# Optimization experiments

Hardware: AMD Instinct MI355X
Metric: run time of the kernel (lower is better)

Reference implementation:

```python
import jax, jax.numpy as jnp
import numpy as np

N = 4096
IN_DIM = 6
HID = 32
HEADS1 = 4
OUT_DIM = 64


def _gat_layer(x, mask, W, a_src, a_dst, b):
    # x: [n, in], W: [in, heads*d], a_src/a_dst: [heads, d], b: [heads*d]
    n = x.shape[0]
    heads, d = a_src.shape
    h = (x @ W).reshape(n, heads, d)                      # [n, heads, d]
    e_src = jnp.einsum('nhd,hd->nh', h, a_src)            # [n, heads]
    e_dst = jnp.einsum('nhd,hd->nh', h, a_dst)            # [n, heads]
    logits = e_src[:, None, :] + e_dst[None, :, :]        # [n, n, heads]
    logits = jax.nn.leaky_relu(logits, negative_slope=0.2)
    logits = jnp.where(mask[:, :, None], logits, jnp.float32(-1e9))
    alpha = jax.nn.softmax(logits, axis=1)                # softmax over j (dim=1)
    # dropout disabled (eval mode reference)
    out = jnp.einsum('ijh,jhd->ihd', alpha, h).reshape(n, heads * d)
    return out + b


def setup_inputs() -> dict:
    key = jax.random.key(0)
    ks = jax.random.split(key, 10)
    x = jax.random.normal(ks[0], (N, IN_DIM), dtype=jnp.float32)
    adj = jax.random.bernoulli(ks[1], 0.01, (N, N)).astype(jnp.float32)
    s = 0.1
    W1 = jax.random.normal(ks[2], (IN_DIM, HEADS1 * HID), dtype=jnp.float32) * s
    a_src1 = jax.random.normal(ks[3], (HEADS1, HID), dtype=jnp.float32) * s
    a_dst1 = jax.random.normal(ks[4], (HEADS1, HID), dtype=jnp.float32) * s
    b1 = jnp.zeros((HEADS1 * HID,), dtype=jnp.float32)
    W2 = jax.random.normal(ks[5], (HEADS1 * HID, OUT_DIM), dtype=jnp.float32) * s
    a_src2 = jax.random.normal(ks[6], (1, OUT_DIM), dtype=jnp.float32) * s
    a_dst2 = jax.random.normal(ks[7], (1, OUT_DIM), dtype=jnp.float32) * s
    b2 = jnp.zeros((OUT_DIM,), dtype=jnp.float32)
    return {'x': x, 'adj': adj, 'W1': W1, 'a_src1': a_src1, 'a_dst1': a_dst1,
            'b1': b1, 'W2': W2, 'a_src2': a_src2, 'a_dst2': a_dst2, 'b2': b2}


def reference(x, adj, W1, a_src1, a_dst1, b1, W2, a_src2, a_dst2, b2):
    n = x.shape[0]
    # add self loops: a = max(a, I), mask = a > 0
    a = jnp.maximum(adj, jnp.eye(n, dtype=adj.dtype))
    mask = a > 0
    h1 = jax.nn.elu(_gat_layer(x, mask, W1, a_src1, a_dst1, b1))
    # dropout disabled (eval mode)
    h2 = _gat_layer(h1, mask, W2, a_src2, a_dst2, b2)
    return h2
```

## Files before the change

### kernel.cpp

```cpp
#include <hip/hip_runtime.h>

#define N 4096
#define IN_DIM 6
#define HID 32
#define HEADS1 4
#define D1 (HEADS1*HID)
#define OUT_DIM 64
#define MAXNB 192

__global__ void kA(const float* __restrict__ x,
                   const float* __restrict__ W1,
                   const float* __restrict__ a_src1,
                   const float* __restrict__ a_dst1,
                   float* __restrict__ hpre,
                   float* __restrict__ es1,
                   float* __restrict__ ed1) {
    int t  = threadIdx.x;
    int r  = t >> 7;
    int tt = t & 127;
    int i  = blockIdx.x * 2 + r;
    __shared__ float xs[2][IN_DIM];
    if (tt < IN_DIM) xs[r][tt] = x[i*IN_DIM + tt];
    __syncthreads();
    float acc = 0.f;
    #pragma unroll
    for (int k = 0; k < IN_DIM; ++k)
        acc += xs[r][k] * W1[k*D1 + tt];
    hpre[(size_t)i*D1 + tt] = acc;
    float ps = acc * a_src1[tt];
    float pd = acc * a_dst1[tt];
    #pragma unroll
    for (int off = 16; off >= 1; off >>= 1) {
        ps += __shfl_xor(ps, off, 64);
        pd += __shfl_xor(pd, off, 64);
    }
    if ((tt & 31) == 0) {
        int h = tt >> 5;
        es1[i*HEADS1 + h] = ps;
        ed1[i*HEADS1 + h] = pd;
    }
}

__global__ void kB(const float* __restrict__ adj,
                   const float* __restrict__ hpre,
                   const float* __restrict__ es1,
                   const float* __restrict__ ed1,
                   const float* __restrict__ b1,
                   const float* __restrict__ W2,
                   const float* __restrict__ a_src2,
                   const float* __restrict__ a_dst2,
                   int* __restrict__ cnt, int* __restrict__ idxg,
                   float* __restrict__ h2pre,
                   float* __restrict__ es2, float* __restrict__ ed2) {
    int i = blockIdx.x;
    int t = threadIdx.x;
    __shared__ int   cL;
    __shared__ int   js[MAXNB];
    __shared__ float lg[HEADS1][MAXNB];
    __shared__ float esi[HEADS1];
    __shared__ float sinv[HEADS1];
    __shared__ float part[128];
    __shared__ float h1s[D1];
    __shared__ float p2s[256];
    if (t == 0) cL = 0;
    if (t < HEADS1) esi[t] = es1[i*HEADS1 + t];
    __syncthreads();

    const float4* row  = (const float4*)(adj + (size_t)i * N);
    const float4* ed1v = (const float4*)ed1;
    for (int k = t; k < N/4; k += 256) {
        float4 v = row[k];
        float f[4] = {v.x, v.y, v.z, v.w};
        #pragma unroll
        for (int q = 0; q < 4; ++q) {
            int j = k*4 + q;
            if (f[q] > 0.f || j == i) {
                int p = atomicAdd(&cL, 1);
                if (p < MAXNB) {
                    js[p] = j;
                    float4 e4 = ed1v[j];
                    float le[4] = {e4.x, e4.y, e4.z, e4.w};
                    #pragma unroll
                    for (int h = 0; h < HEADS1; ++h) {
                        float l = esi[h] + le[h];
                        lg[h][p] = (l > 0.f) ? l : 0.2f*l;
                    }
                }
            }
        }
    }
    __syncthreads();
    int c = min(cL, MAXNB);

    if (t >= 128) {
        if (t == 128) cnt[i] = c;
        for (int p = t - 128; p < c; p += 128) idxg[i*MAXNB + p] = js[p];
    } else {
        int h = t >> 5, lane = t & 31;
        float m = -1e30f;
        for (int p = lane; p < c; p += 32) m = fmaxf(m, lg[h][p]);
        #pragma unroll
        for (int off = 16; off >= 1; off >>= 1) m = fmaxf(m, __shfl_xor(m, off, 64));
        float s = 0.f;
        for (int p = lane; p < c; p += 32) {
            float e = __expf(lg[h][p] - m);
            lg[h][p] = e;
            s += e;
        }
        #pragma unroll
        for (int off = 16; off >= 1; off >>= 1) s += __shfl_xor(s, off, 64);
        if (lane == 0) sinv[h] = 1.f / s;
    }
    __syncthreads();

    int g = t >> 7, tt = t & 127, hh = (t & 127) >> 5;
    float acc = 0.f;
    for (int p = g; p < c; p += 2)
        acc += lg[hh][p] * hpre[(size_t)js[p]*D1 + tt];
    if (g == 1) part[tt] = acc;
    __syncthreads();
    if (g == 0) {
        acc += part[tt];
        float val = acc * sinv[hh] + b1[tt];
        h1s[tt] = (val > 0.f) ? val : expm1f(val);
    }
    __syncthreads();

    int o = t & 63, q = t >> 6;
    float pa = 0.f;
    #pragma unroll
    for (int k = 0; k < 32; ++k) {
        int kk = q*32 + k;
        pa += h1s[kk] * W2[kk*OUT_DIM + o];
    }
    p2s[t] = pa;
    __syncthreads();
    if (t < 64) {
        float h2 = p2s[t] + p2s[t+64] + p2s[t+128] + p2s[t+192];
        h2pre[(size_t)i*OUT_DIM + t] = h2;
        float ps = h2 * a_src2[t];
        float pd = h2 * a_dst2[t];
        #pragma unroll
        for (int off = 32; off >= 1; off >>= 1) {
            ps += __shfl_xor(ps, off, 64);
            pd += __shfl_xor(pd, off, 64);
        }
        if (t == 0) { es2[i] = ps; ed2[i] = pd; }
    }
}

__global__ void kC(const float* __restrict__ h2pre,
                   const float* __restrict__ es2,
                   const float* __restrict__ ed2,
                   const int* __restrict__ cnt,
                   const int* __restrict__ idxg,
                   const float* __restrict__ b2v,
                   float* __restrict__ out) {
    int i = blockIdx.x;
    int t = threadIdx.x;
    int c = cnt[i];
    __shared__ int   js[MAXNB];
    __shared__ float al[MAXNB];
    for (int p = t; p < c; p += 64) js[p] = idxg[i*MAXNB + p];
    __syncthreads();
    float esi = es2[i];
    float m = -1e30f;
    for (int p = t; p < c; p += 64) {
        float l = esi + ed2[js[p]];
        l = (l > 0.f) ? l : 0.2f*l;
        al[p] = l;
        m = fmaxf(m, l);
    }
    #pragma unroll
    for (int off = 32; off >= 1; off >>= 1) m = fmaxf(m, __shfl_xor(m, off, 64));
    __syncthreads();
    float s = 0.f;
    for (int p = t; p < c; p += 64) {
        float e = __expf(al[p] - m);
        al[p] = e;
        s += e;
    }
    #pragma unroll
    for (int off = 32; off >= 1; off >>= 1) s += __shfl_xor(s, off, 64);
    float inv = 1.f / s;
    __syncthreads();
    float acc = 0.f;
    for (int p = 0; p < c; ++p)
        acc += al[p] * h2pre[(size_t)js[p]*OUT_DIM + t];
    out[(size_t)i*OUT_DIM + t] = acc * inv + b2v[t];
}

extern "C" void kernel_launch(void* const* d_in, const int* in_sizes, int n_in,
                              void* d_out, int out_size, void* d_ws, size_t ws_size,
                              hipStream_t stream) {
    const float* x      = (const float*)d_in[0];
    const float* adj    = (const float*)d_in[1];
    const float* W1     = (const float*)d_in[2];
    const float* a_src1 = (const float*)d_in[3];
    const float* a_dst1 = (const float*)d_in[4];
    const float* b1     = (const float*)d_in[5];
    const float* W2     = (const float*)d_in[6];
    const float* a_src2 = (const float*)d_in[7];
    const float* a_dst2 = (const float*)d_in[8];
    const float* b2v    = (const float*)d_in[9];
    float* out = (float*)d_out;

    float* ws    = (float*)d_ws;
    float* hpre  = ws;
    float* h2pre = hpre  + (size_t)N*D1;
    float* es1   = h2pre + (size_t)N*OUT_DIM;
    float* ed1   = es1   + (size_t)N*HEADS1;
    float* es2   = ed1   + (size_t)N*HEADS1;
    float* ed2   = es2   + N;
    int*   cnt   = (int*)(ed2 + N);
    int*   idxg  = cnt + N;

    kA<<<N/2, 256, 0, stream>>>(x, W1, a_src1, a_dst1, hpre, es1, ed1);
    kB<<<N,   256, 0, stream>>>(adj, hpre, es1, ed1, b1, W2, a_src2, a_dst2,
                                cnt, idxg, h2pre, es2, ed2);
    kC<<<N,    64, 0, stream>>>(h2pre, es2, ed2, cnt, idxg, b2v, out);
}
```

Baseline: 148.6 us.

## Process one row per wavefront with ballot compaction and barrier-free softmax

All three kernels are restructured so that each 64-lane wavefront handles one node, with four nodes per block. Block-wide __syncthreads are replaced with wave-local LDS fences. Neighbor compaction now uses ballot/popcount instead of shared atomics, and the adjacency row loads are software-prefetched. Softmax is done in registers with wave shuffles, exponentials are recomputed during aggregation, and W2 is pre-transposed in kA so kB can use vectorized loads. The aim is to cut synchronisation and atomic overhead and raise memory-level parallelism, at the risk of relying on wave-synchronous LDS semantics.

```diff
diff --git a/kernel.cpp b/kernel.cpp
--- a/kernel.cpp
+++ b/kernel.cpp
@@ -2,192 +2,275 @@
 
 #define N 4096
 #define IN_DIM 6
-#define HID 32
 #define HEADS1 4
-#define D1 (HEADS1*HID)
+#define D1 128
 #define OUT_DIM 64
 #define MAXNB 192
 
-__global__ void kA(const float* __restrict__ x,
-                   const float* __restrict__ W1,
-                   const float* __restrict__ a_src1,
-                   const float* __restrict__ a_dst1,
-                   float* __restrict__ hpre,
-                   float* __restrict__ es1,
-                   float* __restrict__ ed1) {
-    int t  = threadIdx.x;
-    int r  = t >> 7;
-    int tt = t & 127;
-    int i  = blockIdx.x * 2 + r;
-    __shared__ float xs[2][IN_DIM];
-    if (tt < IN_DIM) xs[r][tt] = x[i*IN_DIM + tt];
-    __syncthreads();
-    float acc = 0.f;
-    #pragma unroll
-    for (int k = 0; k < IN_DIM; ++k)
-        acc += xs[r][k] * W1[k*D1 + tt];
-    hpre[(size_t)i*D1 + tt] = acc;
-    float ps = acc * a_src1[tt];
-    float pd = acc * a_dst1[tt];
-    #pragma unroll
-    for (int off = 16; off >= 1; off >>= 1) {
+#define WFENCE() do { asm volatile("s_waitcnt lgkmcnt(0)" ::: "memory"); \
+                      __builtin_amdgcn_sched_barrier(0); } while (0)
+
+__device__ __forceinline__ float lrelu(float v) { return v > 0.f ? v : 0.2f * v; }
+__device__ __forceinline__ float selh(float4 v, int h) {
+    return (h == 0) ? v.x : (h == 1) ? v.y : (h == 2) ? v.z : v.w;
+}
+
+__global__ __launch_bounds__(256) void kA(
+    const float* __restrict__ x,  const float* __restrict__ W1,
+    const float* __restrict__ a_src1, const float* __restrict__ a_dst1,
+    const float* __restrict__ W2,
+    float* __restrict__ hpre, float* __restrict__ es1, float* __restrict__ ed1,
+    float* __restrict__ W2T)
+{
+    int w = threadIdx.x >> 6, l = threadIdx.x & 63;
+    int i = blockIdx.x * 4 + w;
+
+    float xv[IN_DIM];
+    #pragma unroll
+    for (int k = 0; k < IN_DIM; ++k) xv[k] = x[i*IN_DIM + k];
+
+    float a0 = 0.f, a1 = 0.f;
+    #pragma unroll
+    for (int k = 0; k < IN_DIM; ++k) {
+        float2 wv = ((const float2*)W1)[k*64 + l];
+        a0 += xv[k] * wv.x;
+        a1 += xv[k] * wv.y;
+    }
+    float2 hv; hv.x = a0; hv.y = a1;
+    ((float2*)hpre)[(size_t)i*64 + l] = hv;
+
+    float2 asv = ((const float2*)a_src1)[l];
+    float2 adv = ((const float2*)a_dst1)[l];
+    float ps = a0*asv.x + a1*asv.y;
+    float pd = a0*adv.x + a1*adv.y;
+    #pragma unroll
+    for (int off = 8; off >= 1; off >>= 1) {
         ps += __shfl_xor(ps, off, 64);
         pd += __shfl_xor(pd, off, 64);
     }
-    if ((tt & 31) == 0) {
-        int h = tt >> 5;
+    if ((l & 15) == 0) {
+        int h = l >> 4;
         es1[i*HEADS1 + h] = ps;
         ed1[i*HEADS1 + h] = pd;
     }
-}
-
-__global__ void kB(const float* __restrict__ adj,
-                   const float* __restrict__ hpre,
-                   const float* __restrict__ es1,
-                   const float* __restrict__ ed1,
-                   const float* __restrict__ b1,
-                   const float* __restrict__ W2,
-                   const float* __restrict__ a_src2,
-                   const float* __restrict__ a_dst2,
-                   int* __restrict__ cnt, int* __restrict__ idxg,
-                   float* __restrict__ h2pre,
-                   float* __restrict__ es2, float* __restrict__ ed2) {
-    int i = blockIdx.x;
-    int t = threadIdx.x;
-    __shared__ int   cL;
-    __shared__ int   js[MAXNB];
-    __shared__ float lg[HEADS1][MAXNB];
-    __shared__ float esi[HEADS1];
-    __shared__ float sinv[HEADS1];
-    __shared__ float part[128];
-    __shared__ float h1s[D1];
-    __shared__ float p2s[256];
-    if (t == 0) cL = 0;
-    if (t < HEADS1) esi[t] = es1[i*HEADS1 + t];
-    __syncthreads();
-
-    const float4* row  = (const float4*)(adj + (size_t)i * N);
-    const float4* ed1v = (const float4*)ed1;
-    for (int k = t; k < N/4; k += 256) {
-        float4 v = row[k];
-        float f[4] = {v.x, v.y, v.z, v.w};
-        #pragma unroll
-        for (int q = 0; q < 4; ++q) {
-            int j = k*4 + q;
-            if (f[q] > 0.f || j == i) {
-                int p = atomicAdd(&cL, 1);
-                if (p < MAXNB) {
-                    js[p] = j;
-                    float4 e4 = ed1v[j];
-                    float le[4] = {e4.x, e4.y, e4.z, e4.w};
-                    #pragma unroll
-                    for (int h = 0; h < HEADS1; ++h) {
-                        float l = esi[h] + le[h];
-                        lg[h][p] = (l > 0.f) ? l : 0.2f*l;
-                    }
+
+    if (blockIdx.x == 0) {
+        for (int idx = threadIdx.x; idx < D1*OUT_DIM; idx += 256) {
+            int k = idx >> 6, o = idx & 63;
+            W2T[o*D1 + k] = W2[idx];
+        }
+    }
+}
+
+__global__ __launch_bounds__(256, 4) void kB(
+    const float* __restrict__ adj,  const float* __restrict__ hpre,
+    const float* __restrict__ es1,  const float* __restrict__ ed1,
+    const float* __restrict__ b1,   const float* __restrict__ W2T,
+    const float* __restrict__ a_src2, const float* __restrict__ a_dst2,
+    int* __restrict__ cnt, int* __restrict__ idxg,
+    float* __restrict__ h2pre, float* __restrict__ es2, float* __restrict__ ed2)
+{
+    __shared__ int   jsS[4][MAXNB];
+    __shared__ float lgS[4][HEADS1][MAXNB];
+    __shared__ float h1S[4][D1];
+    int w = threadIdx.x >> 6, l = threadIdx.x & 63;
+    int i = blockIdx.x * 4 + w;
+    int*   js  = jsS[w];
+    float (*lg)[MAXNB] = lgS[w];
+    float* h1s = h1S[w];
+
+    const float4* row = (const float4*)(adj + (size_t)i * N);
+    unsigned long long lanem = (1ull << l) - 1ull;
+    int base = 0;
+    float4 buf[4];
+    #pragma unroll
+    for (int u = 0; u < 4; ++u) buf[u] = row[l + 64*u];
+    #pragma unroll
+    for (int ch = 0; ch < 4; ++ch) {
+        float4 nbuf[4];
+        if (ch < 3) {
+            #pragma unroll
+            for (int u = 0; u < 4; ++u) nbuf[u] = row[l + 64*u + 256*(ch+1)];
+        }
+        #pragma unroll
+        for (int u = 0; u < 4; ++u) {
+            float fe[4] = {buf[u].x, buf[u].y, buf[u].z, buf[u].w};
+            #pragma unroll
+            for (int e = 0; e < 4; ++e) {
+                int j = (256*ch + 64*u + l)*4 + e;
+                bool pred = (fe[e] > 0.f) || (j == i);
+                unsigned long long mask = __ballot(pred);
+                if (pred) {
+                    int pos = base + (int)__popcll(mask & lanem);
+                    if (pos < MAXNB) js[pos] = j;
                 }
+                base += (int)__popcll(mask);
             }
         }
-    }
-    __syncthreads();
-    int c = min(cL, MAXNB);
-
-    if (t >= 128) {
-        if (t == 128) cnt[i] = c;
-        for (int p = t - 128; p < c; p += 128) idxg[i*MAXNB + p] = js[p];
-    } else {
-        int h = t >> 5, lane = t & 31;
-        float m = -1e30f;
-        for (int p = lane; p < c; p += 32) m = fmaxf(m, lg[h][p]);
-        #pragma unroll
-        for (int off = 16; off >= 1; off >>= 1) m = fmaxf(m, __shfl_xor(m, off, 64));
-        float s = 0.f;
-        for (int p = lane; p < c; p += 32) {
-            float e = __expf(lg[h][p] - m);
-            lg[h][p] = e;
-            s += e;
-        }
-        #pragma unroll
-        for (int off = 16; off >= 1; off >>= 1) s += __shfl_xor(s, off, 64);
-        if (lane == 0) sinv[h] = 1.f / s;
-    }
-    __syncthreads();
-
-    int g = t >> 7, tt = t & 127, hh = (t & 127) >> 5;
-    float acc = 0.f;
-    for (int p = g; p < c; p += 2)
-        acc += lg[hh][p] * hpre[(size_t)js[p]*D1 + tt];
-    if (g == 1) part[tt] = acc;
-    __syncthreads();
-    if (g == 0) {
-        acc += part[tt];
-        float val = acc * sinv[hh] + b1[tt];
-        h1s[tt] = (val > 0.f) ? val : expm1f(val);
-    }
-    __syncthreads();
-
-    int o = t & 63, q = t >> 6;
-    float pa = 0.f;
-    #pragma unroll
-    for (int k = 0; k < 32; ++k) {
-        int kk = q*32 + k;
-        pa += h1s[kk] * W2[kk*OUT_DIM + o];
-    }
-    p2s[t] = pa;
-    __syncthreads();
-    if (t < 64) {
-        float h2 = p2s[t] + p2s[t+64] + p2s[t+128] + p2s[t+192];
-        h2pre[(size_t)i*OUT_DIM + t] = h2;
-        float ps = h2 * a_src2[t];
-        float pd = h2 * a_dst2[t];
-        #pragma unroll
-        for (int off = 32; off >= 1; off >>= 1) {
-            ps += __shfl_xor(ps, off, 64);
-            pd += __shfl_xor(pd, off, 64);
-        }
-        if (t == 0) { es2[i] = ps; ed2[i] = pd; }
-    }
-}
-
-__global__ void kC(const float* __restrict__ h2pre,
-                   const float* __restrict__ es2,
-                   const float* __restrict__ ed2,
-                   const int* __restrict__ cnt,
-                   const int* __restrict__ idxg,
-                   const float* __restrict__ b2v,
-                   float* __restrict__ out) {
-    int i = blockIdx.x;
-    int t = threadIdx.x;
+        if (ch < 3) {
+            #pragma unroll
+            for (int u = 0; u < 4; ++u) buf[u] = nbuf[u];
+        }
+    }
+    int c = min(base, MAXNB);
+    if (l == 0) cnt[i] = c;
+    WFENCE();
+
+    float4 esv = ((const float4*)es1)[i];
+    float4 lr0, lr1, lr2;
+    lr0.x = lr0.y = lr0.z = lr0.w = -1e30f; lr1 = lr0; lr2 = lr0;
+    if (l < c) {
+        int j = js[l];
+        float4 e4 = ((const float4*)ed1)[j];
+        lr0.x = lrelu(esv.x + e4.x); lr0.y = lrelu(esv.y + e4.y);
+        lr0.z = lrelu(esv.z + e4.z); lr0.w = lrelu(esv.w + e4.w);
+        lg[0][l] = lr0.x; lg[1][l] = lr0.y; lg[2][l] = lr0.z; lg[3][l] = lr0.w;
+        idxg[i*MAXNB + l] = j;
+    }
+    if (l + 64 < c) {
+        int p = l + 64, j = js[p];
+        float4 e4 = ((const float4*)ed1)[j];
+        lr1.x = lrelu(esv.x + e4.x); lr1.y = lrelu(esv.y + e4.y);
+        lr1.z = lrelu(esv.z + e4.z); lr1.w = lrelu(esv.w + e4.w);
+        lg[0][p] = lr1.x; lg[1][p] = lr1.y; lg[2][p] = lr1.z; lg[3][p] = lr1.w;
+        idxg[i*MAXNB + p] = j;
+    }
+    if (l + 128 < c) {
+        int p = l + 128, j = js[p];
+        float4 e4 = ((const float4*)ed1)[j];
+        lr2.x = lrelu(esv.x + e4.x); lr2.y = lrelu(esv.y + e4.y);
+        lr2.z = lrelu(esv.z + e4.z); lr2.w = lrelu(esv.w + e4.w);
+        lg[0][p] = lr2.x; lg[1][p] = lr2.y; lg[2][p] = lr2.z; lg[3][p] = lr2.w;
+        idxg[i*MAXNB + p] = j;
+    }
+
+    float4 mm;
+    mm.x = fmaxf(lr0.x, fmaxf(lr1.x, lr2.x));
+    mm.y = fmaxf(lr0.y, fmaxf(lr1.y, lr2.y));
+    mm.z = fmaxf(lr0.z, fmaxf(lr1.z, lr2.z));
+    mm.w = fmaxf(lr0.w, fmaxf(lr1.w, lr2.w));
+    #pragma unroll
+    for (int off = 32; off >= 1; off >>= 1) {
+        mm.x = fmaxf(mm.x, __shfl_xor(mm.x, off, 64));
+        mm.y = fmaxf(mm.y, __shfl_xor(mm.y, off, 64));
+        mm.z = fmaxf(mm.z, __shfl_xor(mm.z, off, 64));
+        mm.w = fmaxf(mm.w, __shfl_xor(mm.w, off, 64));
+    }
+    float4 ss;
+    ss.x = __expf(lr0.x-mm.x) + __expf(lr1.x-mm.x) + __expf(lr2.x-mm.x);
+    ss.y = __expf(lr0.y-mm.y) + __expf(lr1.y-mm.y) + __expf(lr2.y-mm.y);
+    ss.z = __expf(lr0.z-mm.z) + __expf(lr1.z-mm.z) + __expf(lr2.z-mm.z);
+    ss.w = __expf(lr0.w-mm.w) + __expf(lr1.w-mm.w) + __expf(lr2.w-mm.w);
+    #pragma unroll
+    for (int off = 32; off >= 1; off >>= 1) {
+        ss.x += __shfl_xor(ss.x, off, 64);
+        ss.y += __shfl_xor(ss.y, off, 64);
+        ss.z += __shfl_xor(ss.z, off, 64);
+        ss.w += __shfl_xor(ss.w, off, 64);
+    }
+    WFENCE();
+
+    int hl = l >> 4;
+    float m   = selh(mm, hl);
+    float inv = 1.f / selh(ss, hl);
+    const float2* hp2 = (const float2*)hpre;
+    float ax = 0.f, ay = 0.f;
+    int p = 0;
+    for (; p + 8 <= c; p += 8) {
+        int   jj[8]; float ww[8];
+        #pragma unroll
+        for (int u = 0; u < 8; ++u) jj[u] = js[p+u];
+        #pragma unroll
+        for (int u = 0; u < 8; ++u) ww[u] = __expf(lg[hl][p+u] - m);
+        #pragma unroll
+        for (int u = 0; u < 8; ++u) {
+            float2 v = hp2[(size_t)jj[u]*64 + l];
+            ax += ww[u]*v.x; ay += ww[u]*v.y;
+        }
+    }
+    for (; p < c; ++p) {
+        float wv = __expf(lg[hl][p] - m);
+        float2 v = hp2[(size_t)js[p]*64 + l];
+        ax += wv*v.x; ay += wv*v.y;
+    }
+    float2 bv = ((const float2*)b1)[l];
+    float v0 = ax*inv + bv.x, v1 = ay*inv + bv.y;
+    v0 = (v0 > 0.f) ? v0 : expm1f(v0);
+    v1 = (v1 > 0.f) ? v1 : expm1f(v1);
+    { float2 hw; hw.x = v0; hw.y = v1; *(float2*)(h1s + 2*l) = hw; }
+    WFENCE();
+
+    const float4* wrow = (const float4*)(W2T + (size_t)l*D1);
+    float h2 = 0.f;
+    #pragma unroll 8
+    for (int k4 = 0; k4 < 32; ++k4) {
+        float4 wv = wrow[k4];
+        float4 hvv = *(const float4*)(h1s + k4*4);
+        h2 += wv.x*hvv.x + wv.y*hvv.y + wv.z*hvv.z + wv.w*hvv.w;
+    }
+    h2pre[(size_t)i*OUT_DIM + l] = h2;
+    float ps = h2 * a_src2[l];
+    float pd = h2 * a_dst2[l];
+    #pragma unroll
+    for (int off = 32; off >= 1; off >>= 1) {
+        ps += __shfl_xor(ps, off, 64);
+        pd += __shfl_xor(pd, off, 64);
+    }
+    if (l == 0) { es2[i] = ps; ed2[i] = pd; }
+}
+
+__global__ __launch_bounds__(256, 6) void kC(
+    const float* __restrict__ h2pre, const float* __restrict__ es2,
+    const float* __restrict__ ed2,   const int* __restrict__ cnt,
+    const int* __restrict__ idxg,    const float* __restrict__ b2v,
+    float* __restrict__ out)
+{
+    __shared__ int   jsS[4][MAXNB];
+    __shared__ float alS[4][MAXNB];
+    int w = threadIdx.x >> 6, l = threadIdx.x & 63;
+    int i = blockIdx.x * 4 + w;
+    int*   js = jsS[w];
+    float* al = alS[w];
     int c = cnt[i];
-    __shared__ int   js[MAXNB];
-    __shared__ float al[MAXNB];
-    for (int p = t; p < c; p += 64) js[p] = idxg[i*MAXNB + p];
-    __syncthreads();
     float esi = es2[i];
-    float m = -1e30f;
-    for (int p = t; p < c; p += 64) {
-        float l = esi + ed2[js[p]];
-        l = (l > 0.f) ? l : 0.2f*l;
-        al[p] = l;
-        m = fmaxf(m, l);
-    }
+
+    float l0 = -1e30f, l1 = -1e30f, l2 = -1e30f;
+    if (l < c) {
+        int j = idxg[i*MAXNB + l];            js[l] = j;
+        float v = lrelu(esi + ed2[j]);        al[l] = v;  l0 = v;
+    }
+    if (l + 64 < c) {
+        int p = l + 64, j = idxg[i*MAXNB + p]; js[p] = j;
+        float v = lrelu(esi + ed2[j]);         al[p] = v;  l1 = v;
+    }
+    if (l + 128 < c) {
+        int p = l + 128, j = idxg[i*MAXNB + p]; js[p] = j;
+        float v = lrelu(esi + ed2[j]);          al[p] = v;  l2 = v;
+    }
+    float m = fmaxf(l0, fmaxf(l1, l2));
     #pragma unroll
     for (int off = 32; off >= 1; off >>= 1) m = fmaxf(m, __shfl_xor(m, off, 64));
-    __syncthreads();
-    float s = 0.f;
-    for (int p = t; p < c; p += 64) {
-        float e = __expf(al[p] - m);
-        al[p] = e;
-        s += e;
-    }
+    float s = __expf(l0-m) + __expf(l1-m) + __expf(l2-m);
     #pragma unroll
     for (int off = 32; off >= 1; off >>= 1) s += __shfl_xor(s, off, 64);
     float inv = 1.f / s;
-    __syncthreads();
+    WFENCE();
+
     float acc = 0.f;
-    for (int p = 0; p < c; ++p)
-        acc += al[p] * h2pre[(size_t)js[p]*OUT_DIM + t];
-    out[(size_t)i*OUT_DIM + t] = acc * inv + b2v[t];
+    int p = 0;
+    for (; p + 8 <= c; p += 8) {
+        int   jj[8]; float ww[8];
+        #pragma unroll
+        for (int u = 0; u < 8; ++u) jj[u] = js[p+u];
+        #pragma unroll
+        for (int u = 0; u < 8; ++u) ww[u] = __expf(al[p+u] - m);
+        #pragma unroll
+        for (int u = 0; u < 8; ++u)
+            acc += ww[u] * h2pre[(size_t)jj[u]*OUT_DIM + l];
+    }
+    for (; p < c; ++p)
+        acc += __expf(al[p] - m) * h2pre[(size_t)js[p]*OUT_DIM + l];
+    out[(size_t)i*OUT_DIM + l] = acc*inv + b2v[l];
 }
 
 extern "C" void kernel_launch(void* const* d_in, const int* in_sizes, int n_in,
@@ -212,11 +295,12 @@
     float* ed1   = es1   + (size_t)N*HEADS1;
     float* es2   = ed1   + (size_t)N*HEADS1;
     float* ed2   = es2   + N;
-    int*   cnt   = (int*)(ed2 + N);
+    float* W2T   = ed2   + N;
+    int*   cnt   = (int*)(W2T + OUT_DIM*D1);
     int*   idxg  = cnt + N;
 
-    kA<<<N/2, 256, 0, stream>>>(x, W1, a_src1, a_dst1, hpre, es1, ed1);
-    kB<<<N,   256, 0, stream>>>(adj, hpre, es1, ed1, b1, W2, a_src2, a_dst2,
+    kA<<<N/4, 256, 0, stream>>>(x, W1, a_src1, a_dst1, W2, hpre, es1, ed1, W2T);
+    kB<<<N/4, 256, 0, stream>>>(adj, hpre, es1, ed1, b1, W2T, a_src2, a_dst2,
                                 cnt, idxg, h2pre, es2, ed2);
-    kC<<<N,    64, 0, stream>>>(h2pre, es2, ed2, cnt, idxg, b2v, out);
-}
+    kC<<<N/4, 256, 0, stream>>>(h2pre, es2, ed2, cnt, idxg, b2v, out);
+}
```

New measurement: 147.4 us. About the same (-0.8%).
